# Performance work log

Hardware: AMD Instinct MI355X
Metric: run time of the kernel (lower is better)

Reference implementation:

```python
import jax, jax.numpy as jnp
import numpy as np

BATCH, SEQ, DIM = 4, 4096, 1024


def setup_inputs() -> dict:
    key = jax.random.key(0)
    ks = jax.random.split(key, 7)
    return {
        "x": jax.random.normal(ks[0], (BATCH, SEQ, DIM), dtype=jnp.float32),
        "phazor_re": jax.random.normal(ks[1], (DIM,), dtype=jnp.float32),
        "phazor_im": jax.random.normal(ks[2], (DIM,), dtype=jnp.float32),
        "phazor_init_re": jax.random.normal(ks[3], (DIM,), dtype=jnp.float32),
        "phazor_init_im": jax.random.normal(ks[4], (DIM,), dtype=jnp.float32),
        "last_conv_re": jax.random.normal(ks[5], (BATCH, DIM), dtype=jnp.float32),
        "last_conv_im": jax.random.normal(ks[6], (BATCH, DIM), dtype=jnp.float32),
    }


def reference(x, phazor_re, phazor_im, phazor_init_re, phazor_init_im,
              last_conv_re, last_conv_im):
    L = x.shape[1]
    phazor_p = phazor_re + 1j * phazor_im                      # raw param (dim,)
    phazor_init = phazor_init_re + 1j * phazor_init_im          # (dim,)
    last_conv = last_conv_re + 1j * last_conv_im                # (batch, dim)

    mag = jnp.abs(phazor_p)
    phazor = phazor_p / mag * jnp.exp(-mag)                     # (dim,) |phazor|<1
    t = jnp.arange(L)[:, None]                                  # (L,1)
    phazor_prog = jnp.power(phazor[None, :], t)                 # (L, dim) = phazor^t
    filt = phazor_prog * phazor_init[None, :]                   # (L, dim)

    filt_fft = jnp.fft.fft(filt, n=2 * L, axis=0)               # (2L, dim)
    x_fft = jnp.fft.fft(x.astype(jnp.complex64), n=2 * L, axis=1)  # (B, 2L, dim)
    conv = jnp.fft.ifft(filt_fft[None] * x_fft, axis=1)[:, :L]  # (B, L, dim)

    # add decayed initial state: last_conv * phazor^(t+1)
    conv = conv + last_conv[:, None, :] * phazor_prog[None] * phazor[None, None, :]
    return conv.real
```

## Files before the change

kernel.cpp:

```cpp
#include <hip/hip_runtime.h>


#define BB 4
#define LL 4096
#define DD 1024
#define CHUNK 16
#define KK 256
#define SEG 32
#define NSEG 8

__device__ __forceinline__ void phazor_of(float pr, float pi, float& ar, float& ai) {
    float mag = sqrtf(pr * pr + pi * pi);
    float s = expf(-mag) / mag;
    ar = pr * s;
    ai = pi * s;
}

__device__ __forceinline__ void csq(float& r, float& i) {
    float nr = r * r - i * i;
    i = 2.f * r * i;
    r = nr;
}

__global__ __launch_bounds__(256, 4) void spiral_p1(
    const float* __restrict__ x,
    const float* __restrict__ p_re, const float* __restrict__ p_im,
    const float* __restrict__ in_re, const float* __restrict__ in_im,
    float2* __restrict__ S)
{
    int tid = blockIdx.x * 256 + threadIdx.x;
    int dq = tid & (DD / 4 - 1);
    int k  = (tid >> 8) & (KK - 1);
    int b  = tid >> 16;
    int d0 = dq * 4;

    float4 prv = *(const float4*)(p_re + d0);
    float4 piv = *(const float4*)(p_im + d0);
    float4 brv = *(const float4*)(in_re + d0);
    float4 biv = *(const float4*)(in_im + d0);
    float ar[4], ai[4];
    float br[4] = {brv.x, brv.y, brv.z, brv.w};
    float bi[4] = {biv.x, biv.y, biv.z, biv.w};
    {
        float prs[4] = {prv.x, prv.y, prv.z, prv.w};
        float pis[4] = {piv.x, piv.y, piv.z, piv.w};
#pragma unroll
        for (int q = 0; q < 4; ++q) phazor_of(prs[q], pis[q], ar[q], ai[q]);
    }

    float sr[4] = {0.f, 0.f, 0.f, 0.f};
    float si[4] = {0.f, 0.f, 0.f, 0.f};
    const float* xp = x + ((size_t)(b * LL + k * CHUNK) * DD + d0);

#pragma unroll
    for (int t0 = 0; t0 < CHUNK; t0 += 8) {
        float4 xv[8];
#pragma unroll
        for (int j = 0; j < 8; ++j)
            xv[j] = *(const float4*)(xp + (size_t)(t0 + j) * DD);
#pragma unroll
        for (int j = 0; j < 8; ++j) {
            float xs[4] = {xv[j].x, xv[j].y, xv[j].z, xv[j].w};
#pragma unroll
            for (int q = 0; q < 4; ++q) {
                float nr = fmaf(ar[q], sr[q], fmaf(-ai[q], si[q], br[q] * xs[q]));
                float ni = fmaf(ar[q], si[q], fmaf( ai[q], sr[q], bi[q] * xs[q]));
                sr[q] = nr; si[q] = ni;
            }
        }
    }

    float2* Sp = S + ((size_t)(b * KK + k) * DD + d0);
#pragma unroll
    for (int q = 0; q < 4; ++q) Sp[q] = make_float2(sr[q], si[q]);
}

__global__ __launch_bounds__(128) void spiral_p2a(
    const float* __restrict__ p_re, const float* __restrict__ p_im,
    const float2* __restrict__ S,
    float2* __restrict__ R, float2* __restrict__ T)
{
    int gt  = blockIdx.x * 128 + threadIdx.x;
    int d   = gt & (DD - 1);
    int seg = (gt >> 10) & (NSEG - 1);
    int bb  = gt >> 13;

    float qr, qi;
    phazor_of(p_re[d], p_im[d], qr, qi);
#pragma unroll
    for (int i = 0; i < 4; ++i) csq(qr, qi);

    const int kk0 = seg * SEG;
    const float2* Sc = S + ((size_t)bb * KK * DD + d);
    float2*       Rc = R + ((size_t)bb * KK * DD + d);

    float2 buf[8];
#pragma unroll
    for (int j = 0; j < 8; ++j) buf[j] = Sc[(size_t)(kk0 + j) * DD];

    float cr = 0.f, ci = 0.f;
    for (int i = 0; i < SEG; i += 8) {
#pragma unroll
        for (int j = 0; j < 8; ++j) {
            Rc[(size_t)(kk0 + i + j) * DD] = make_float2(cr, ci);
            float2 s = buf[j];
            int kn = i + j + 8;
            buf[j] = Sc[(size_t)(kk0 + (kn < SEG ? kn : SEG - 1)) * DD];
            float nr = fmaf(qr, cr, fmaf(-qi, ci, s.x));
            float ni = fmaf(qr, ci, fmaf( qi, cr, s.y));
            cr = nr; ci = ni;
        }
    }
    T[((size_t)bb * NSEG + seg) * DD + d] = make_float2(cr, ci);
}

__global__ __launch_bounds__(128) void spiral_p2b(
    const float* __restrict__ p_re, const float* __restrict__ p_im,
    const float* __restrict__ lc_re, const float* __restrict__ lc_im,
    const float2* __restrict__ T,
    float2* __restrict__ segC)
{
    int gt = blockIdx.x * 128 + threadIdx.x;
    int d  = gt & (DD - 1);
    int bb = gt >> 10;

    float qr, qi;
    phazor_of(p_re[d], p_im[d], qr, qi);
#pragma unroll
    for (int i = 0; i < 9; ++i) csq(qr, qi);

    float2 tb[NSEG];
#pragma unroll
    for (int s = 0; s < NSEG; ++s) tb[s] = T[((size_t)bb * NSEG + s) * DD + d];

    float cr = lc_re[bb * DD + d];
    float ci = lc_im[bb * DD + d];
#pragma unroll
    for (int s = 0; s < NSEG; ++s) {
        segC[((size_t)bb * NSEG + s) * DD + d] = make_float2(cr, ci);
        float nr = fmaf(qr, cr, fmaf(-qi, ci, tb[s].x));
        float ni = fmaf(qr, ci, fmaf( qi, cr, tb[s].y));
        cr = nr; ci = ni;
    }
}

__global__ __launch_bounds__(256, 4) void spiral_p3(
    const float* __restrict__ x,
    const float* __restrict__ p_re, const float* __restrict__ p_im,
    const float* __restrict__ in_re, const float* __restrict__ in_im,
    const float2* __restrict__ R, const float2* __restrict__ segC,
    float* __restrict__ out)
{
    int tid = blockIdx.x * 256 + threadIdx.x;
    int dq = tid & (DD / 4 - 1);
    int k  = (tid >> 8) & (KK - 1);
    int b  = tid >> 16;
    int d0 = dq * 4;
    int rel = k & (SEG - 1);
    int seg = k >> 5;

    float4 prv = *(const float4*)(p_re + d0);
    float4 piv = *(const float4*)(p_im + d0);
    float4 brv = *(const float4*)(in_re + d0);
    float4 biv = *(const float4*)(in_im + d0);
    float ar[4], ai[4];
    float br[4] = {brv.x, brv.y, brv.z, brv.w};
    float bi[4] = {biv.x, biv.y, biv.z, biv.w};
    {
        float prs[4] = {prv.x, prv.y, prv.z, prv.w};
        float pis[4] = {piv.x, piv.y, piv.z, piv.w};
#pragma unroll
        for (int q = 0; q < 4; ++q) phazor_of(prs[q], pis[q], ar[q], ai[q]);
    }

    float cr[4], ci[4];
    {
        const float2* Rp = R    + ((size_t)(b * KK + k) * DD + d0);
        const float2* Gp = segC + ((size_t)(b * NSEG + seg) * DD + d0);
#pragma unroll
        for (int q = 0; q < 4; ++q) {
            float qdr = ar[q], qdi = ai[q];
#pragma unroll
            for (int i = 0; i < 4; ++i) csq(qdr, qdi);
            float pr = 1.f, pi = 0.f;
            float bpr = qdr, bpi = qdi;
#pragma unroll
            for (int bit = 0; bit < 5; ++bit) {
                if ((rel >> bit) & 1) {
                    float nr = pr * bpr - pi * bpi;
                    pi = pr * bpi + pi * bpr;
                    pr = nr;
                }
                csq(bpr, bpi);
            }
            float2 r = Rp[q];
            float2 g = Gp[q];
            cr[q] = r.x + pr * g.x - pi * g.y;
            ci[q] = r.y + pr * g.y + pi * g.x;
        }
    }

    const size_t base = (size_t)(b * LL + k * CHUNK) * DD + d0;
    const float* xp = x + base;
    float* op = out + base;

#pragma unroll
    for (int t0 = 0; t0 < CHUNK; t0 += 8) {
        float4 xv[8];
#pragma unroll
        for (int j = 0; j < 8; ++j)
            xv[j] = *(const float4*)(xp + (size_t)(t0 + j) * DD);
#pragma unroll
        for (int j = 0; j < 8; ++j) {
            float xs[4] = {xv[j].x, xv[j].y, xv[j].z, xv[j].w};
            float os[4];
#pragma unroll
            for (int q = 0; q < 4; ++q) {
                float nr = fmaf(ar[q], cr[q], fmaf(-ai[q], ci[q], br[q] * xs[q]));
                float ni = fmaf(ar[q], ci[q], fmaf( ai[q], cr[q], bi[q] * xs[q]));
                cr[q] = nr; ci[q] = ni;
                os[q] = nr;
            }
            *(float4*)(op + (size_t)(t0 + j) * DD) = make_float4(os[0], os[1], os[2], os[3]);
        }
    }
}

extern "C" void kernel_launch(void* const* d_in, const int* in_sizes, int n_in,
                              void* d_out, int out_size, void* d_ws, size_t ws_size,
                              hipStream_t stream) {
    const float* x      = (const float*)d_in[0];
    const float* p_re   = (const float*)d_in[1];
    const float* p_im   = (const float*)d_in[2];
    const float* pin_re = (const float*)d_in[3];
    const float* pin_im = (const float*)d_in[4];
    const float* lc_re  = (const float*)d_in[5];
    const float* lc_im  = (const float*)d_in[6];
    float* out = (float*)d_out;

    char* ws = (char*)d_ws;
    float2* S    = (float2*)(ws);
    float2* R    = (float2*)(ws + (size_t)8  * 1024 * 1024);
    float2* T    = (float2*)(ws + (size_t)16 * 1024 * 1024);
    float2* segC = (float2*)(ws + (size_t)16 * 1024 * 1024 + 256 * 1024);

    spiral_p1 <<<dim3(1024), dim3(256), 0, stream>>>(x, p_re, p_im, pin_re, pin_im, S);
    spiral_p2a<<<dim3(256),  dim3(128), 0, stream>>>(p_re, p_im, S, R, T);
    spiral_p2b<<<dim3(32),   dim3(128), 0, stream>>>(p_re, p_im, lc_re, lc_im, T, segC);
    spiral_p3 <<<dim3(1024), dim3(256), 0, stream>>>(x, p_re, p_im, pin_re, pin_im, R, segC, out);
}
```

Measured before the change: 142.8 us.

## Fold segment-carry scan into output kernel and vectorize partial-state stores

Removes the small sequential kernel that scanned the per-segment totals. Each output thread now recomputes its segment's starting carry from last_conv and the segment totals T, running up to seven complex FMA steps per lane. This trades one kernel launch and a dependent round trip through memory for redundant per-thread work and extra T reads. Separately, the chunk partial-state store in the first kernel is packed into two float4 writes instead of four float2 writes.

```diff
diff --git a/kernel.cpp b/kernel.cpp
--- a/kernel.cpp
+++ b/kernel.cpp
@@ -70,9 +70,9 @@
         }
     }
 
-    float2* Sp = S + ((size_t)(b * KK + k) * DD + d0);
-#pragma unroll
-    for (int q = 0; q < 4; ++q) Sp[q] = make_float2(sr[q], si[q]);
+    float4* Sp = (float4*)(S + ((size_t)(b * KK + k) * DD + d0));
+    Sp[0] = make_float4(sr[0], si[0], sr[1], si[1]);
+    Sp[1] = make_float4(sr[2], si[2], sr[3], si[3]);
 }
 
 __global__ __launch_bounds__(128) void spiral_p2a(
@@ -114,41 +114,12 @@
     T[((size_t)bb * NSEG + seg) * DD + d] = make_float2(cr, ci);
 }
 
-__global__ __launch_bounds__(128) void spiral_p2b(
-    const float* __restrict__ p_re, const float* __restrict__ p_im,
-    const float* __restrict__ lc_re, const float* __restrict__ lc_im,
-    const float2* __restrict__ T,
-    float2* __restrict__ segC)
-{
-    int gt = blockIdx.x * 128 + threadIdx.x;
-    int d  = gt & (DD - 1);
-    int bb = gt >> 10;
-
-    float qr, qi;
-    phazor_of(p_re[d], p_im[d], qr, qi);
-#pragma unroll
-    for (int i = 0; i < 9; ++i) csq(qr, qi);
-
-    float2 tb[NSEG];
-#pragma unroll
-    for (int s = 0; s < NSEG; ++s) tb[s] = T[((size_t)bb * NSEG + s) * DD + d];
-
-    float cr = lc_re[bb * DD + d];
-    float ci = lc_im[bb * DD + d];
-#pragma unroll
-    for (int s = 0; s < NSEG; ++s) {
-        segC[((size_t)bb * NSEG + s) * DD + d] = make_float2(cr, ci);
-        float nr = fmaf(qr, cr, fmaf(-qi, ci, tb[s].x));
-        float ni = fmaf(qr, ci, fmaf( qi, cr, tb[s].y));
-        cr = nr; ci = ni;
-    }
-}
-
 __global__ __launch_bounds__(256, 4) void spiral_p3(
     const float* __restrict__ x,
     const float* __restrict__ p_re, const float* __restrict__ p_im,
     const float* __restrict__ in_re, const float* __restrict__ in_im,
-    const float2* __restrict__ R, const float2* __restrict__ segC,
+    const float* __restrict__ lc_re, const float* __restrict__ lc_im,
+    const float2* __restrict__ R, const float2* __restrict__ T,
     float* __restrict__ out)
 {
     int tid = blockIdx.x * 256 + threadIdx.x;
@@ -173,10 +144,34 @@
         for (int q = 0; q < 4; ++q) phazor_of(prs[q], pis[q], ar[q], ai[q]);
     }
 
+    float gr[4], gi[4];
+    {
+        float4 lrv = *(const float4*)(lc_re + b * DD + d0);
+        float4 liv = *(const float4*)(lc_im + b * DD + d0);
+        gr[0] = lrv.x; gr[1] = lrv.y; gr[2] = lrv.z; gr[3] = lrv.w;
+        gi[0] = liv.x; gi[1] = liv.y; gi[2] = liv.z; gi[3] = liv.w;
+        float Qr[4], Qi[4];
+#pragma unroll
+        for (int q = 0; q < 4; ++q) {
+            Qr[q] = ar[q]; Qi[q] = ai[q];
+#pragma unroll
+            for (int i = 0; i < 9; ++i) csq(Qr[q], Qi[q]);
+        }
+        for (int s = 0; s < seg; ++s) {
+            const float2* Tp = T + ((size_t)(b * NSEG + s) * DD + d0);
+#pragma unroll
+            for (int q = 0; q < 4; ++q) {
+                float2 t = Tp[q];
+                float nr = fmaf(Qr[q], gr[q], fmaf(-Qi[q], gi[q], t.x));
+                float ni = fmaf(Qr[q], gi[q], fmaf( Qi[q], gr[q], t.y));
+                gr[q] = nr; gi[q] = ni;
+            }
+        }
+    }
+
     float cr[4], ci[4];
     {
-        const float2* Rp = R    + ((size_t)(b * KK + k) * DD + d0);
-        const float2* Gp = segC + ((size_t)(b * NSEG + seg) * DD + d0);
+        const float2* Rp = R + ((size_t)(b * KK + k) * DD + d0);
 #pragma unroll
         for (int q = 0; q < 4; ++q) {
             float qdr = ar[q], qdi = ai[q];
@@ -194,9 +189,8 @@
                 csq(bpr, bpi);
             }
             float2 r = Rp[q];
-            float2 g = Gp[q];
-            cr[q] = r.x + pr * g.x - pi * g.y;
-            ci[q] = r.y + pr * g.y + pi * g.x;
+            cr[q] = r.x + pr * gr[q] - pi * gi[q];
+            ci[q] = r.y + pr * gi[q] + pi * gr[q];
         }
     }
 
@@ -239,13 +233,12 @@
     float* out = (float*)d_out;
 
     char* ws = (char*)d_ws;
-    float2* S    = (float2*)(ws);
-    float2* R    = (float2*)(ws + (size_t)8  * 1024 * 1024);
-    float2* T    = (float2*)(ws + (size_t)16 * 1024 * 1024);
-    float2* segC = (float2*)(ws + (size_t)16 * 1024 * 1024 + 256 * 1024);
+    float2* S = (float2*)(ws);
+    float2* R = (float2*)(ws + (size_t)8  * 1024 * 1024);
+    float2* T = (float2*)(ws + (size_t)16 * 1024 * 1024);
 
     spiral_p1 <<<dim3(1024), dim3(256), 0, stream>>>(x, p_re, p_im, pin_re, pin_im, S);
     spiral_p2a<<<dim3(256),  dim3(128), 0, stream>>>(p_re, p_im, S, R, T);
-    spiral_p2b<<<dim3(32),   dim3(128), 0, stream>>>(p_re, p_im, lc_re, lc_im, T, segC);
-    spiral_p3 <<<dim3(1024), dim3(256), 0, stream>>>(x, p_re, p_im, pin_re, pin_im, R, segC, out);
-}
+    spiral_p3 <<<dim3(1024), dim3(256), 0, stream>>>(x, p_re, p_im, pin_re, pin_im,
+                                                     lc_re, lc_im, R, T, out);
+}
```

Result: no change. 141.3 us (-1.0%).
